# Kernel tuning notes

Hardware: AMD Instinct MI355X
Metric: run time of the kernel (lower is better)

Reference implementation:

```python
import jax, jax.numpy as jnp
import numpy as np

ALPHA = 0.1  # LeakyReLU negative slope
F_OUT = 128

def _leaky(x):
    return jnp.where(x >= 0, x, ALPHA * x)

def setup_inputs() -> dict:
    key = jax.random.key(0)
    ks = jax.random.split(key, 12)
    B, N, F_IN = 4, 4096, 128
    q = jax.random.normal(ks[0], (B, N, F_IN), jnp.float32)
    k = jax.random.normal(ks[1], (B, N, F_IN), jnp.float32)
    v = jax.random.normal(ks[2], (B, N, F_IN), jnp.float32)
    adj = jax.random.randint(ks[3], (B, N, N), 0, 2, jnp.int32)
    s = 1.0 / np.sqrt(F_IN)
    Wq_w = jax.random.uniform(ks[4], (F_OUT, F_IN), jnp.float32, -s, s)
    Wq_b = jax.random.uniform(ks[5], (F_OUT,), jnp.float32, -s, s)
    Wk_w = jax.random.uniform(ks[6], (F_OUT, F_IN), jnp.float32, -s, s)
    Wk_b = jax.random.uniform(ks[7], (F_OUT,), jnp.float32, -s, s)
    Wv_w = jax.random.uniform(ks[8], (F_OUT, F_IN), jnp.float32, -s, s)
    Wv_b = jax.random.uniform(ks[9], (F_OUT,), jnp.float32, -s, s)
    # xavier_uniform with gain=1.414 on (2F,1)
    lim = 1.414 * np.sqrt(6.0 / (2 * F_OUT + 1))
    a = jax.random.uniform(ks[10], (2 * F_OUT, 1), jnp.float32, -lim, lim)
    so = 1.0 / np.sqrt(F_OUT)
    Wo_w = jax.random.uniform(ks[11], (F_OUT, F_OUT), jnp.float32, -so, so)
    return {"q": q, "k": k, "v": v, "adj": adj, "Wq_w": Wq_w, "Wq_b": Wq_b,
            "Wk_w": Wk_w, "Wk_b": Wk_b, "Wv_w": Wv_w, "Wv_b": Wv_b,
            "a": a, "Wo_w": Wo_w}

def reference(q, k, v, adj, Wq_w, Wq_b, Wk_w, Wk_b, Wv_w, Wv_b, a, Wo_w):
    qp = q @ Wq_w.T + Wq_b                      # (B,N,F)
    kp = k @ Wk_w.T + Wk_b
    vp = v @ Wv_w.T + Wv_b
    Wh1 = qp @ a[:F_OUT]                        # (B,N,1)
    Wh2 = kp @ a[F_OUT:]                        # (B,N,1)
    e = _leaky(Wh1 + jnp.swapaxes(Wh2, 1, 2))   # (B,N,N)
    e = jnp.where(adj > 0, e, jnp.float32(-1e9))
    att = jax.nn.softmax(e, axis=-1)
    h = jnp.einsum('bnm,bmf->bnf', att, vp)     # (B,N,F)
    return _leaky(h @ Wo_w.T)
```

## Files before the change

kernel.cpp:

```cpp
#include <hip/hip_runtime.h>


constexpr int B = 4, N = 4096, F = 128;
constexpr int BN = B * N;
constexpr int BK = 64;
constexpr int SPLITS = 2;
constexpr int JC = N / SPLITS;
constexpr int NIT = JC / BK;
#define ALPHA 0.1f

using float4v = __attribute__((ext_vector_type(4))) float;
using short8 = __attribute__((ext_vector_type(8))) short;

__device__ __forceinline__ float leaky(float x) { return x >= 0.f ? x : ALPHA * x; }
__device__ __forceinline__ unsigned short f2bf(float x) {
    unsigned u = __float_as_uint(x);
    u = (u + 0x7FFFu + ((u >> 16) & 1u)) >> 16;
    return (unsigned short)u;
}
__device__ __forceinline__ unsigned pack_bf2(float lo, float hi) {
    unsigned a = __float_as_uint(lo), b2 = __float_as_uint(hi);
    a = a + 0x7FFFu + ((a >> 16) & 1u);
    b2 = b2 + 0x7FFFu + ((b2 >> 16) & 1u);
    return __builtin_amdgcn_perm(b2, a, 0x07060302u);
}

__global__ void k_prep(const float* __restrict__ Wq_w, const float* __restrict__ Wq_b,
                       const float* __restrict__ Wk_w, const float* __restrict__ Wk_b,
                       const float* __restrict__ a, float* __restrict__ c1,
                       float* __restrict__ c2, float* __restrict__ d12) {
    __shared__ float as[2 * F];
    __shared__ float red[2 * F];
    int t = threadIdx.x;
    as[t] = a[t];
    __syncthreads();
    int f = t & 127;
    const float* W = (t < F) ? Wq_w : Wk_w;
    const float* ao = (t < F) ? as : as + F;
    float s = 0.f;
#pragma unroll 8
    for (int o = 0; o < F; o++) s = fmaf(W[o * F + f], ao[o], s);
    if (t < F) c1[f] = s; else c2[f] = s;
    red[t] = (t < F) ? Wq_b[f] * as[f] : Wk_b[f] * as[F + f];
    __syncthreads();
    for (int st = 64; st > 0; st >>= 1) {
        if (f < st) red[t] += red[t + st];
        __syncthreads();
    }
    if (t == 0) d12[0] = red[0];
    if (t == F) d12[1] = red[F];
}

__global__ void k_wh(const float* __restrict__ q, const float* __restrict__ k,
                     const float* __restrict__ c1, const float* __restrict__ c2,
                     const float* __restrict__ d12,
                     float* __restrict__ Wh1, float* __restrict__ Wh2) {
    __shared__ float c1s[F], c2s[F];
    int t = threadIdx.x;
    if (t < F) c1s[t] = c1[t]; else c2s[t - F] = c2[t - F];
    __syncthreads();
    int row = blockIdx.x * 8 + (t >> 5);
    int lane = t & 31;
    float4 q4 = reinterpret_cast<const float4*>(q)[row * 32 + lane];
    float4 k4 = reinterpret_cast<const float4*>(k)[row * 32 + lane];
    float s1 = q4.x * c1s[lane * 4 + 0] + q4.y * c1s[lane * 4 + 1] +
               q4.z * c1s[lane * 4 + 2] + q4.w * c1s[lane * 4 + 3];
    float s2 = k4.x * c2s[lane * 4 + 0] + k4.y * c2s[lane * 4 + 1] +
               k4.z * c2s[lane * 4 + 2] + k4.w * c2s[lane * 4 + 3];
    for (int m = 16; m > 0; m >>= 1) { s1 += __shfl_xor(s1, m); s2 += __shfl_xor(s2, m); }
    if (lane == 0) { Wh1[row] = s1 + d12[0]; Wh2[row] = s2 + d12[1]; }
}

__global__ void k_max2(const float* __restrict__ Wh2, float* __restrict__ M2) {
    int b = blockIdx.x, t = threadIdx.x;
    float m = -1e30f;
    for (int i = t; i < N; i += 256) m = fmaxf(m, Wh2[b * N + i]);
    __shared__ float red[256];
    red[t] = m;
    __syncthreads();
    for (int s = 128; s > 0; s >>= 1) { if (t < s) red[t] = fmaxf(red[t], red[t + s]); __syncthreads(); }
    if (t == 0) M2[b] = red[0];
}

__global__ void k_tab(const float* __restrict__ Wh1, const float* __restrict__ Wh2,
                      const float* __restrict__ M2,
                      float* __restrict__ P1, float* __restrict__ Q1,
                      float* __restrict__ P2, float* __restrict__ Q2) {
    int i = blockIdx.x * 256 + threadIdx.x;
    int b = i >> 12;
    float w1 = Wh1[i], w2 = Wh2[i];
    float mi = leaky(w1 + M2[b]);
    P1[i] = __expf(w1 - mi);
    Q1[i] = __expf(ALPHA * w1 - mi);
    P2[i] = __expf(w2);
    Q2[i] = __expf(ALPHA * w2);
}

__global__ __launch_bounds__(256) void k_vp(const float* __restrict__ v,
                                            const float* __restrict__ Wv_w,
                                            const float* __restrict__ Wv_b,
                                            unsigned short* __restrict__ vpT) {
    __shared__ float vs[32][F];
    __shared__ float Ws[F][129];
    __shared__ unsigned short ts[F][40];
    int t = threadIdx.x;
    int row0g = blockIdx.x * 32;
    int b = row0g >> 12;
    int row0 = row0g & (N - 1);
    {
        const float4* src = reinterpret_cast<const float4*>(v + row0g * F);
        float4* dst = reinterpret_cast<float4*>(&vs[0][0]);
#pragma unroll
        for (int u = 0; u < 4; u++) dst[u * 256 + t] = src[u * 256 + t];
    }
    {
        const float4* src = reinterpret_cast<const float4*>(Wv_w);
#pragma unroll
        for (int u = 0; u < 16; u++) {
            int unit = u * 256 + t;
            int r = unit >> 5, s = unit & 31;
            float4 val = src[unit];
            Ws[r][s * 4 + 0] = val.x; Ws[r][s * 4 + 1] = val.y;
            Ws[r][s * 4 + 2] = val.z; Ws[r][s * 4 + 3] = val.w;
        }
    }
    int f = t & 127, g = t >> 7;
    float bias = Wv_b[f];
    __syncthreads();
    float acc[16];
#pragma unroll
    for (int r = 0; r < 16; r++) acc[r] = bias;
    for (int kk = 0; kk < F; kk++) {
        float wk = Ws[f][kk];
#pragma unroll
        for (int r = 0; r < 16; r++) acc[r] = fmaf(vs[g * 16 + r][kk], wk, acc[r]);
    }
#pragma unroll
    for (int r = 0; r < 16; r++) ts[f][g * 16 + r] = f2bf(acc[r]);
    __syncthreads();
    int fr = t >> 1, hseg = t & 1;
    uint4 d0 = *reinterpret_cast<uint4*>(&ts[fr][hseg * 16]);
    uint4 d1 = *reinterpret_cast<uint4*>(&ts[fr][hseg * 16 + 8]);
    unsigned short* dst = vpT + ((size_t)(b * F + fr) * N + row0 + hseg * 16);
    *reinterpret_cast<uint4*>(dst) = d0;
    *reinterpret_cast<uint4*>(dst + 8) = d1;
}

__global__ __launch_bounds__(256, 2) void k_attn(
    const unsigned short* __restrict__ vpT, const int* __restrict__ adj,
    const float* __restrict__ Wh1, const float* __restrict__ P1, const float* __restrict__ Q1,
    const float* __restrict__ P2, const float* __restrict__ Q2, const float* __restrict__ Wh2,
    float* __restrict__ h_part, float* __restrict__ den_part) {
    int t = threadIdx.x;
    int idx = blockIdx.x;
    int split = idx & (SPLITS - 1);
    int tile = (idx / SPLITS) & 127;
    int b = idx / (SPLITS * 128);
    int i0 = tile * 32;
    int jb0 = split * JC;
    int widx = t >> 6, lane = t & 63, m = lane & 15, q = lane >> 4;
    int rt = widx >> 1;
    int kh = widx & 1;
    int r0 = i0 + rt * 16;

    int gi0 = b * N + r0 + m;
    float p1a = P1[gi0], q1a = Q1[gi0], t1a = -Wh1[gi0];

    int jo = jb0 + kh * 32 + q * 8;
    const unsigned short* bfb = vpT + ((size_t)(b * F + m)) * N + jo;
    const int* adjb = adj + (size_t)gi0 * N + jo;
    const float* W2b = Wh2 + (size_t)b * N + jo;
    const float* P2b = P2 + (size_t)b * N + jo;
    const float* Q2b = Q2 + (size_t)b * N + jo;

    float4v acc0[8];
#pragma unroll
    for (int nt = 0; nt < 8; nt++) acc0[nt] = (float4v){0.f, 0.f, 0.f, 0.f};
    float den0 = 0.f;

    auto body = [&](int it, const int4& a0, const int4& a1) {
        const float* w = W2b + it * BK;
        float4 x2a = *reinterpret_cast<const float4*>(w);
        float4 x2b = *reinterpret_cast<const float4*>(w + 4);
        const float* p = P2b + it * BK;
        float4 p2a = *reinterpret_cast<const float4*>(p);
        float4 p2b = *reinterpret_cast<const float4*>(p + 4);
        const float* qq = Q2b + it * BK;
        float4 q2a = *reinterpret_cast<const float4*>(qq);
        float4 q2b = *reinterpret_cast<const float4*>(qq + 4);
        const unsigned short* vr = bfb + it * BK;
        short8 bf0 = *reinterpret_cast<const short8*>(vr);
        short8 bf1 = *reinterpret_cast<const short8*>(vr + (size_t)1 * 16 * N);
        short8 bf2 = *reinterpret_cast<const short8*>(vr + (size_t)2 * 16 * N);
        short8 bf3 = *reinterpret_cast<const short8*>(vr + (size_t)3 * 16 * N);
        short8 bf4 = *reinterpret_cast<const short8*>(vr + (size_t)4 * 16 * N);
        short8 bf5 = *reinterpret_cast<const short8*>(vr + (size_t)5 * 16 * N);
        short8 bf6 = *reinterpret_cast<const short8*>(vr + (size_t)6 * 16 * N);
        short8 bf7 = *reinterpret_cast<const short8*>(vr + (size_t)7 * 16 * N);

        float w0 = a0.x ? ((x2a.x >= t1a) ? p1a * p2a.x : q1a * q2a.x) : 0.f;
        float w1 = a0.y ? ((x2a.y >= t1a) ? p1a * p2a.y : q1a * q2a.y) : 0.f;
        float w2 = a0.z ? ((x2a.z >= t1a) ? p1a * p2a.z : q1a * q2a.z) : 0.f;
        float w3 = a0.w ? ((x2a.w >= t1a) ? p1a * p2a.w : q1a * q2a.w) : 0.f;
        float w4 = a1.x ? ((x2b.x >= t1a) ? p1a * p2b.x : q1a * q2b.x) : 0.f;
        float w5 = a1.y ? ((x2b.y >= t1a) ? p1a * p2b.y : q1a * q2b.y) : 0.f;
        float w6 = a1.z ? ((x2b.z >= t1a) ? p1a * p2b.z : q1a * q2b.z) : 0.f;
        float w7 = a1.w ? ((x2b.w >= t1a) ? p1a * p2b.w : q1a * q2b.w) : 0.f;
        den0 += ((w0 + w1) + (w2 + w3)) + ((w4 + w5) + (w6 + w7));
        union { short8 s; uint4 u; } af;
        af.u.x = pack_bf2(w0, w1); af.u.y = pack_bf2(w2, w3);
        af.u.z = pack_bf2(w4, w5); af.u.w = pack_bf2(w6, w7);

        acc0[0] = __builtin_amdgcn_mfma_f32_16x16x32_bf16(af.s, bf0, acc0[0], 0, 0, 0);
        acc0[1] = __builtin_amdgcn_mfma_f32_16x16x32_bf16(af.s, bf1, acc0[1], 0, 0, 0);
        acc0[2] = __builtin_amdgcn_mfma_f32_16x16x32_bf16(af.s, bf2, acc0[2], 0, 0, 0);
        acc0[3] = __builtin_amdgcn_mfma_f32_16x16x32_bf16(af.s, bf3, acc0[3], 0, 0, 0);
        acc0[4] = __builtin_amdgcn_mfma_f32_16x16x32_bf16(af.s, bf4, acc0[4], 0, 0, 0);
        acc0[5] = __builtin_amdgcn_mfma_f32_16x16x32_bf16(af.s, bf5, acc0[5], 0, 0, 0);
        acc0[6] = __builtin_amdgcn_mfma_f32_16x16x32_bf16(af.s, bf6, acc0[6], 0, 0, 0);
        acc0[7] = __builtin_amdgcn_mfma_f32_16x16x32_bf16(af.s, bf7, acc0[7], 0, 0, 0);
    };

    int4 aA0, aA1, aB0, aB1;
    {
        const int* p0 = adjb;
        aA0 = *reinterpret_cast<const int4*>(p0);
        aA1 = *reinterpret_cast<const int4*>(p0 + 4);
        const int* p1 = adjb + BK;
        aB0 = *reinterpret_cast<const int4*>(p1);
        aB1 = *reinterpret_cast<const int4*>(p1 + 4);
    }
#pragma unroll 1
    for (int ith = 0; ith < NIT / 2; ith++) {
        int it = ith * 2;
        body(it, aA0, aA1);
        if (it + 2 < NIT) {
            const int* p = adjb + (size_t)(it + 2) * BK;
            aA0 = *reinterpret_cast<const int4*>(p);
            aA1 = *reinterpret_cast<const int4*>(p + 4);
        }
        body(it + 1, aB0, aB1);
        if (it + 3 < NIT) {
            const int* p = adjb + (size_t)(it + 3) * BK;
            aB0 = *reinterpret_cast<const int4*>(p);
            aB1 = *reinterpret_cast<const int4*>(p + 4);
        }
    }

    den0 += __shfl_xor(den0, 16);
    den0 += __shfl_xor(den0, 32);
    int pidx = split * 2 + kh;
    float* dp = den_part + (size_t)pidx * BN;
    if (lane < 16) dp[gi0] = den0;
    float* hp = h_part + (size_t)pidx * BN * F;
    int orow0 = b * N + i0 + rt * 16 + q * 4;
#pragma unroll
    for (int nt = 0; nt < 8; nt++)
#pragma unroll
        for (int r = 0; r < 4; r++)
            hp[(size_t)(orow0 + r) * F + nt * 16 + m] = acc0[nt][r];
}

__global__ __launch_bounds__(256) void k_out(const float* __restrict__ h_part,
                                             const float* __restrict__ den_part,
                                             const float* __restrict__ Wo_w,
                                             float* __restrict__ out) {
    __shared__ float hs[32][F];
    __shared__ float Ws[F][129];
    int t = threadIdx.x;
    int row0 = blockIdx.x * 32;
    {
        const float4* src = reinterpret_cast<const float4*>(Wo_w);
#pragma unroll
        for (int u = 0; u < 16; u++) {
            int unit = u * 256 + t;
            int r = unit >> 5, s = unit & 31;
            float4 val = src[unit];
            Ws[r][s * 4 + 0] = val.x; Ws[r][s * 4 + 1] = val.y;
            Ws[r][s * 4 + 2] = val.z; Ws[r][s * 4 + 3] = val.w;
        }
    }
#pragma unroll
    for (int u = 0; u < 4; u++) {
        int unit = u * 256 + t;
        int r = unit >> 5, s = unit & 31;
        size_t off = (size_t)(row0 + r) * F + s * 4;
        float4 h0 = *reinterpret_cast<const float4*>(h_part + off);
        float4 h1 = *reinterpret_cast<const float4*>(h_part + (size_t)BN * F + off);
        float4 h2 = *reinterpret_cast<const float4*>(h_part + (size_t)2 * BN * F + off);
        float4 h3 = *reinterpret_cast<const float4*>(h_part + (size_t)3 * BN * F + off);
        float dsum = den_part[row0 + r] + den_part[BN + row0 + r] +
                     den_part[2 * BN + row0 + r] + den_part[3 * BN + row0 + r];
        float inv = 1.f / dsum;
        hs[r][s * 4 + 0] = (h0.x + h1.x + h2.x + h3.x) * inv;
        hs[r][s * 4 + 1] = (h0.y + h1.y + h2.y + h3.y) * inv;
        hs[r][s * 4 + 2] = (h0.z + h1.z + h2.z + h3.z) * inv;
        hs[r][s * 4 + 3] = (h0.w + h1.w + h2.w + h3.w) * inv;
    }
    __syncthreads();
    int f = t & 127, g = t >> 7;
    float acc[16];
#pragma unroll
    for (int r = 0; r < 16; r++) acc[r] = 0.f;
    for (int kk = 0; kk < F; kk++) {
        float wk = Ws[f][kk];
#pragma unroll
        for (int r = 0; r < 16; r++) acc[r] = fmaf(hs[g * 16 + r][kk], wk, acc[r]);
    }
#pragma unroll
    for (int r = 0; r < 16; r++) out[(size_t)(row0 + g * 16 + r) * F + f] = leaky(acc[r]);
}

extern "C" void kernel_launch(void* const* d_in, const int* in_sizes, int n_in,
                              void* d_out, int out_size, void* d_ws, size_t ws_size,
                              hipStream_t stream) {
    const float* q    = (const float*)d_in[0];
    const float* k    = (const float*)d_in[1];
    const float* v    = (const float*)d_in[2];
    const int*   adj  = (const int*)d_in[3];
    const float* Wq_w = (const float*)d_in[4];
    const float* Wq_b = (const float*)d_in[5];
    const float* Wk_w = (const float*)d_in[6];
    const float* Wk_b = (const float*)d_in[7];
    const float* Wv_w = (const float*)d_in[8];
    const float* Wv_b = (const float*)d_in[9];
    const float* a    = (const float*)d_in[10];
    const float* Wo_w = (const float*)d_in[11];
    float* out = (float*)d_out;
    float* ws = (float*)d_ws;

    unsigned short* vpT = (unsigned short*)ws;
    float* h_part   = ws + BN * F / 2;
    float* den_part = h_part + (size_t)4 * BN * F;
    float* Wh1 = den_part + 4 * BN;
    float* Wh2 = Wh1 + BN;
    float* P1  = Wh2 + BN;
    float* Q1  = P1 + BN;
    float* P2  = Q1 + BN;
    float* Q2  = P2 + BN;
    float* c1  = Q2 + BN;
    float* c2  = c1 + F;
    float* d12 = c2 + F;
    float* M2  = d12 + 2;

    k_prep<<<1, 256, 0, stream>>>(Wq_w, Wq_b, Wk_w, Wk_b, a, c1, c2, d12);
    k_wh<<<BN / 8, 256, 0, stream>>>(q, k, c1, c2, d12, Wh1, Wh2);
    k_max2<<<B, 256, 0, stream>>>(Wh2, M2);
    k_tab<<<BN / 256, 256, 0, stream>>>(Wh1, Wh2, M2, P1, Q1, P2, Q2);
    k_vp<<<BN / 32, 256, 0, stream>>>(v, Wv_w, Wv_b, vpT);
    k_attn<<<B * 128 * SPLITS, 256, 0, stream>>>(vpT, adj, Wh1, P1, Q1, P2, Q2, Wh2,
                                                 h_part, den_part);
    k_out<<<BN / 32, 256, 0, stream>>>(h_part, den_part, Wo_w, out);
}
```

Measured before the change: 570.4 us.

## Stage V tile through double-buffered LDS and raise occupancy hint

The attention kernel now loads each 128x64 bf16 V tile cooperatively with coalesced 16-byte loads into a double-buffered shared-memory array, then reads MFMA B operands from LDS. Before, each wave loaded its strided B fragments directly from global memory, and waves sharing the same V columns duplicated that traffic. Register prefetch of the next stage overlaps with compute, at the cost of a block-wide barrier per step and extra LDS traffic. The launch bound is raised to 4 blocks per CU, which caps register use and may cause spills.

```diff
diff --git a/kernel.cpp b/kernel.cpp
--- a/kernel.cpp
+++ b/kernel.cpp
@@ -146,11 +146,12 @@
     *reinterpret_cast<uint4*>(dst + 8) = d1;
 }
 
-__global__ __launch_bounds__(256, 2) void k_attn(
+__global__ __launch_bounds__(256, 4) void k_attn(
     const unsigned short* __restrict__ vpT, const int* __restrict__ adj,
     const float* __restrict__ Wh1, const float* __restrict__ P1, const float* __restrict__ Q1,
     const float* __restrict__ P2, const float* __restrict__ Q2, const float* __restrict__ Wh2,
     float* __restrict__ h_part, float* __restrict__ den_part) {
+    __shared__ __align__(16) unsigned short bs[2][F][72];
     int t = threadIdx.x;
     int idx = blockIdx.x;
     int split = idx & (SPLITS - 1);
@@ -167,7 +168,7 @@
     float p1a = P1[gi0], q1a = Q1[gi0], t1a = -Wh1[gi0];
 
     int jo = jb0 + kh * 32 + q * 8;
-    const unsigned short* bfb = vpT + ((size_t)(b * F + m)) * N + jo;
+    const unsigned short* vb = vpT + (size_t)b * F * N + jb0;
     const int* adjb = adj + (size_t)gi0 * N + jo;
     const float* W2b = Wh2 + (size_t)b * N + jo;
     const float* P2b = P2 + (size_t)b * N + jo;
@@ -178,7 +179,25 @@
     for (int nt = 0; nt < 8; nt++) acc0[nt] = (float4v){0.f, 0.f, 0.f, 0.f};
     float den0 = 0.f;
 
-    auto body = [&](int it, const int4& a0, const int4& a1) {
+    uint4 sreg[4];
+    auto load_stage = [&](int it) {
+#pragma unroll
+        for (int u = 0; u < 4; u++) {
+            int unit = u * 256 + t;
+            int r = unit >> 3, s = unit & 7;
+            sreg[u] = *reinterpret_cast<const uint4*>(vb + (size_t)r * N + it * BK + s * 8);
+        }
+    };
+    auto write_stage = [&](int pb) {
+#pragma unroll
+        for (int u = 0; u < 4; u++) {
+            int unit = u * 256 + t;
+            int r = unit >> 3, s = unit & 7;
+            *reinterpret_cast<uint4*>(&bs[pb][r][s * 8]) = sreg[u];
+        }
+    };
+
+    auto body = [&](int it, const int4& a0, const int4& a1, int pb) {
         const float* w = W2b + it * BK;
         float4 x2a = *reinterpret_cast<const float4*>(w);
         float4 x2b = *reinterpret_cast<const float4*>(w + 4);
@@ -188,15 +207,6 @@
         const float* qq = Q2b + it * BK;
         float4 q2a = *reinterpret_cast<const float4*>(qq);
         float4 q2b = *reinterpret_cast<const float4*>(qq + 4);
-        const unsigned short* vr = bfb + it * BK;
-        short8 bf0 = *reinterpret_cast<const short8*>(vr);
-        short8 bf1 = *reinterpret_cast<const short8*>(vr + (size_t)1 * 16 * N);
-        short8 bf2 = *reinterpret_cast<const short8*>(vr + (size_t)2 * 16 * N);
-        short8 bf3 = *reinterpret_cast<const short8*>(vr + (size_t)3 * 16 * N);
-        short8 bf4 = *reinterpret_cast<const short8*>(vr + (size_t)4 * 16 * N);
-        short8 bf5 = *reinterpret_cast<const short8*>(vr + (size_t)5 * 16 * N);
-        short8 bf6 = *reinterpret_cast<const short8*>(vr + (size_t)6 * 16 * N);
-        short8 bf7 = *reinterpret_cast<const short8*>(vr + (size_t)7 * 16 * N);
 
         float w0 = a0.x ? ((x2a.x >= t1a) ? p1a * p2a.x : q1a * q2a.x) : 0.f;
         float w1 = a0.y ? ((x2a.y >= t1a) ? p1a * p2a.y : q1a * q2a.y) : 0.f;
@@ -211,17 +221,15 @@
         af.u.x = pack_bf2(w0, w1); af.u.y = pack_bf2(w2, w3);
         af.u.z = pack_bf2(w4, w5); af.u.w = pack_bf2(w6, w7);
 
-        acc0[0] = __builtin_amdgcn_mfma_f32_16x16x32_bf16(af.s, bf0, acc0[0], 0, 0, 0);
-        acc0[1] = __builtin_amdgcn_mfma_f32_16x16x32_bf16(af.s, bf1, acc0[1], 0, 0, 0);
-        acc0[2] = __builtin_amdgcn_mfma_f32_16x16x32_bf16(af.s, bf2, acc0[2], 0, 0, 0);
-        acc0[3] = __builtin_amdgcn_mfma_f32_16x16x32_bf16(af.s, bf3, acc0[3], 0, 0, 0);
-        acc0[4] = __builtin_amdgcn_mfma_f32_16x16x32_bf16(af.s, bf4, acc0[4], 0, 0, 0);
-        acc0[5] = __builtin_amdgcn_mfma_f32_16x16x32_bf16(af.s, bf5, acc0[5], 0, 0, 0);
-        acc0[6] = __builtin_amdgcn_mfma_f32_16x16x32_bf16(af.s, bf6, acc0[6], 0, 0, 0);
-        acc0[7] = __builtin_amdgcn_mfma_f32_16x16x32_bf16(af.s, bf7, acc0[7], 0, 0, 0);
+#pragma unroll
+        for (int nt = 0; nt < 8; nt++) {
+            short8 bf = *reinterpret_cast<const short8*>(&bs[pb][nt * 16 + m][kh * 32 + q * 8]);
+            acc0[nt] = __builtin_amdgcn_mfma_f32_16x16x32_bf16(af.s, bf, acc0[nt], 0, 0, 0);
+        }
     };
 
     int4 aA0, aA1, aB0, aB1;
+    load_stage(0);
     {
         const int* p0 = adjb;
         aA0 = *reinterpret_cast<const int4*>(p0);
@@ -230,21 +238,30 @@
         aB0 = *reinterpret_cast<const int4*>(p1);
         aB1 = *reinterpret_cast<const int4*>(p1 + 4);
     }
+    write_stage(0);
+    __syncthreads();
+
 #pragma unroll 1
     for (int ith = 0; ith < NIT / 2; ith++) {
         int it = ith * 2;
-        body(it, aA0, aA1);
+        if (it + 1 < NIT) load_stage(it + 1);
+        body(it, aA0, aA1, 0);
         if (it + 2 < NIT) {
             const int* p = adjb + (size_t)(it + 2) * BK;
             aA0 = *reinterpret_cast<const int4*>(p);
             aA1 = *reinterpret_cast<const int4*>(p + 4);
         }
-        body(it + 1, aB0, aB1);
+        if (it + 1 < NIT) write_stage(1);
+        __syncthreads();
+        if (it + 2 < NIT) load_stage(it + 2);
+        body(it + 1, aB0, aB1, 1);
         if (it + 3 < NIT) {
             const int* p = adjb + (size_t)(it + 3) * BK;
             aB0 = *reinterpret_cast<const int4*>(p);
             aB1 = *reinterpret_cast<const int4*>(p + 4);
         }
+        if (it + 2 < NIT) write_stage(0);
+        __syncthreads();
     }
 
     den0 += __shfl_xor(den0, 16);
```

Measured after the change: 630.6 us. 10.6% more time.
